# Kernel tuning notes

Measured on AMD Instinct MI355X. Metric: run time of the kernel, lower is better.

Reference implementation:

```python
import jax, jax.numpy as jnp
import numpy as np

B, L, FEAT = 128, 64, 2048   # batch, num image regions, cnn feature dim
T = 48                        # max_seq_len
EMB, UNITS, VOCAB = 256, 512, 5000


def setup_inputs() -> dict:
    key = jax.random.key(0)
    ks = jax.random.split(key, 16)
    s = 0.02
    inp = {
        "img_tensor": jax.random.normal(ks[0], (B, L, FEAT), dtype=jnp.float32),
        "target": jax.random.randint(ks[1], (B, T), 0, VOCAB, dtype=jnp.int32),
        # CNN_Encoder fc: 2048 -> 256
        "W_fc": jax.random.normal(ks[2], (FEAT, EMB), dtype=jnp.float32) * s,
        "b_fc": jnp.zeros((EMB,), jnp.float32),
        # BahdanauAttention
        "W1": jax.random.normal(ks[3], (EMB, UNITS), dtype=jnp.float32) * s,
        "b1": jnp.zeros((UNITS,), jnp.float32),
        "W2": jax.random.normal(ks[4], (UNITS, UNITS), dtype=jnp.float32) * s,
        "b2": jnp.zeros((UNITS,), jnp.float32),
        "V": jax.random.normal(ks[5], (UNITS, 1), dtype=jnp.float32) * s,
        "bV": jnp.zeros((1,), jnp.float32),
        # Decoder embedding
        "emb": jax.random.normal(ks[6], (VOCAB, EMB), dtype=jnp.float32) * s,
        # Keras GRU (reset_after=True): input dim = EMB + UNITS? no: concat(context EMB=256, emb 256) = 512
        "gru_k": jax.random.normal(ks[7], (EMB + EMB, 3 * UNITS), dtype=jnp.float32) * s,
        "gru_rk": jax.random.normal(ks[8], (UNITS, 3 * UNITS), dtype=jnp.float32) * s,
        "gru_b": jnp.zeros((2, 3 * UNITS), jnp.float32),
        # fc1: units->units, fc2: units->vocab
        "fc1_w": jax.random.normal(ks[9], (UNITS, UNITS), dtype=jnp.float32) * s,
        "fc1_b": jnp.zeros((UNITS,), jnp.float32),
        "fc2_w": jax.random.normal(ks[10], (UNITS, VOCAB), dtype=jnp.float32) * s,
        "fc2_b": jnp.zeros((VOCAB,), jnp.float32),
    }
    return inp


def reference(img_tensor, target, W_fc, b_fc, W1, b1, W2, b2, V, bV, emb,
              gru_k, gru_rk, gru_b, fc1_w, fc1_b, fc2_w, fc2_b):
    # CNN encoder: (B, L, EMB)
    features = jax.nn.relu(jnp.einsum('blf,fe->ble', img_tensor, W_fc) + b_fc)
    # Precompute W1(features): invariant across timesteps
    feat_w1 = jnp.einsum('ble,eu->blu', features, W1) + b1  # (B, L, UNITS)

    def step(carry, tok_next):
        hidden, tok = carry
        # Bahdanau attention
        hid_w2 = hidden @ W2 + b2                         # (B, UNITS)
        score = jnp.tanh(feat_w1 + hid_w2[:, None, :])    # (B, L, UNITS)
        logits_attn = jnp.einsum('blu,uo->blo', score, V) + bV  # (B, L, 1)
        attn = jax.nn.softmax(logits_attn, axis=1)
        context = jnp.sum(attn * features, axis=1)        # (B, EMB)
        # Embed previous token, concat with context (seq len 1)
        x = jnp.concatenate([context, emb[tok]], axis=-1)  # (B, 2*EMB)
        # GRU step. NOTE: the original TF code calls self.gru(x) with NO
        # initial_state, so the GRU state is zeros at every timestep.
        h0 = jnp.zeros_like(hidden)
        mx = x @ gru_k + gru_b[0]                          # (B, 3U)
        mh = h0 @ gru_rk + gru_b[1]                        # (B, 3U)
        xz, xr, xh = jnp.split(mx, 3, axis=-1)
        rz, rr, rh = jnp.split(mh, 3, axis=-1)
        z = jax.nn.sigmoid(xz + rz)
        r = jax.nn.sigmoid(xr + rr)
        hh = jnp.tanh(xh + r * rh)
        state = z * h0 + (1.0 - z) * hh                    # (B, UNITS)
        # fc1 -> fc2 logits
        out = state @ fc1_w + fc1_b
        logits = out @ fc2_w + fc2_b                       # (B, VOCAB)
        return (state, tok_next), logits

    batch = target.shape[0]
    hidden0 = jnp.zeros((batch, UNITS), dtype=features.dtype)
    tok0 = jnp.ones((batch,), dtype=target.dtype)          # start token id 1
    xs = jnp.transpose(target[:, 1:], (1, 0))              # (T-1, B)
    _, logits_t = jax.lax.scan(step, (hidden0, tok0), xs)  # (T-1, B, VOCAB)
    return jnp.transpose(logits_t, (1, 0, 2))              # (B, T-1, VOCAB)
```

## Files before the change

kernel.cpp:

```cpp
#include <hip/hip_runtime.h>

typedef __attribute__((ext_vector_type(8))) short short8;
typedef __attribute__((ext_vector_type(4))) float f32x4;

__device__ __forceinline__ float bf2f(ushort u) {
  union { unsigned int i; float f; } x; x.i = ((unsigned int)u) << 16; return x.f;
}
__device__ __forceinline__ ushort f2bf(float f) {
  union { float f; unsigned int i; } x; x.f = f;
  unsigned int i = x.i + 0x7fffu + ((x.i >> 16) & 1u);
  return (ushort)(i >> 16);
}
__device__ __forceinline__ float blo(unsigned int u) {
  union { unsigned int i; float f; } x; x.i = u << 16; return x.f;
}
__device__ __forceinline__ float bhi(unsigned int u) {
  union { unsigned int i; float f; } x; x.i = u & 0xffff0000u; return x.f;
}
__device__ __forceinline__ float fast_tanh(float x) {
  x = fminf(fmaxf(x, -15.f), 15.f);
  float e = __expf(2.f * x);
  return __fdividef(e - 1.f, e + 1.f);
}
__device__ __forceinline__ float sigm(float x) { return 1.f / (1.f + __expf(-x)); }

__global__ void transpose_f2b(const float* __restrict__ in, ushort* __restrict__ out,
                              int R, int C) {
  __shared__ ushort tile[32][33];
  int c0 = blockIdx.x * 32, r0 = blockIdx.y * 32;
  int tx = threadIdx.x, ty = threadIdx.y;
  for (int i = 0; i < 32; i += 8) {
    int r = r0 + ty + i, c = c0 + tx;
    if (r < R && c < C) tile[ty + i][tx] = f2bf(in[(size_t)r * C + c]);
  }
  __syncthreads();
  for (int i = 0; i < 32; i += 8) {
    int c = c0 + ty + i, r = r0 + tx;
    if (r < R && c < C) out[(size_t)c * R + r] = tile[tx][ty + i];
  }
}

__global__ void embed_gather(const int* __restrict__ target, const float* __restrict__ emb,
                             ushort* __restrict__ embA) {
  int m = blockIdx.x;
  int t = m >> 7, b = m & 127;
  int tok = (t == 0) ? 1 : target[b * 48 + t];
  embA[(size_t)m * 256 + threadIdx.x] = f2bf(emb[(size_t)tok * 256 + threadIdx.x]);
}

__global__ __launch_bounds__(256) void gemm128(
    const void* __restrict__ Ap, const ushort* __restrict__ BT,
    const float* __restrict__ bias, void* __restrict__ Cout,
    int M, int N, int K, int NrowsB, int bstride, int flags) {
  __shared__ ushort lA[128 * 32];
  __shared__ ushort lB[128 * 32];
  int tid = threadIdx.x;
  int wave = tid >> 6, lane = tid & 63;
  int q = lane >> 4, l16 = lane & 15;
  int wr = wave >> 1, wc = wave & 1;
  int m0 = blockIdx.y * 128, n0 = blockIdx.x * 128;
  f32x4 acc[4][4];
#pragma unroll
  for (int i = 0; i < 4; ++i)
#pragma unroll
    for (int j = 0; j < 4; ++j) acc[i][j] = (f32x4){0.f, 0.f, 0.f, 0.f};
  int r0 = tid >> 2, cc0 = (tid & 3) * 8;
  int r1 = r0 + 64, cc1 = cc0;
  int rb0 = n0 + r0; if (rb0 >= NrowsB) rb0 = NrowsB - 1;
  int rb1 = n0 + r1; if (rb1 >= NrowsB) rb1 = NrowsB - 1;
  for (int k = 0; k < K; k += 32) {
    short8 va0, va1, vb0, vb1;
    if (flags & 8) {
      const float* s0 = (const float*)Ap + (size_t)(m0 + r0) * K + k + cc0;
      const float* s1 = (const float*)Ap + (size_t)(m0 + r1) * K + k + cc1;
      short8 t0, t1;
#pragma unroll
      for (int e = 0; e < 8; ++e) { t0[e] = (short)f2bf(s0[e]); t1[e] = (short)f2bf(s1[e]); }
      va0 = t0; va1 = t1;
    } else {
      va0 = *(const short8*)((const ushort*)Ap + (size_t)(m0 + r0) * K + k + cc0);
      va1 = *(const short8*)((const ushort*)Ap + (size_t)(m0 + r1) * K + k + cc1);
    }
    vb0 = *(const short8*)(BT + (size_t)rb0 * bstride + k + cc0);
    vb1 = *(const short8*)(BT + (size_t)rb1 * bstride + k + cc1);
    __syncthreads();
    *(short8*)&lA[r0 * 32 + cc0] = va0;
    *(short8*)&lA[r1 * 32 + cc1] = va1;
    *(short8*)&lB[r0 * 32 + cc0] = vb0;
    *(short8*)&lB[r1 * 32 + cc1] = vb1;
    __syncthreads();
    short8 af[4], bfr[4];
#pragma unroll
    for (int i = 0; i < 4; ++i)
      af[i] = *(const short8*)&lA[(wr * 64 + i * 16 + l16) * 32 + q * 8];
#pragma unroll
    for (int j = 0; j < 4; ++j)
      bfr[j] = *(const short8*)&lB[(wc * 64 + j * 16 + l16) * 32 + q * 8];
#pragma unroll
    for (int i = 0; i < 4; ++i)
#pragma unroll
      for (int j = 0; j < 4; ++j)
        acc[i][j] = __builtin_amdgcn_mfma_f32_16x16x32_bf16(af[i], bfr[j], acc[i][j], 0, 0, 0);
  }
#pragma unroll
  for (int i = 0; i < 4; ++i)
#pragma unroll
    for (int j = 0; j < 4; ++j)
#pragma unroll
      for (int r = 0; r < 4; ++r) {
        int gr = m0 + wr * 64 + i * 16 + q * 4 + r;
        int gc = n0 + wc * 64 + j * 16 + l16;
        if (gc >= N) continue;
        float v = acc[i][j][r];
        if (bias) v += bias[gc];
        if (flags & 1) v = fmaxf(v, 0.f);
        size_t orow = (size_t)gr;
        if (flags & 4) { int t = gr >> 7, bb = gr & 127; orow = (size_t)bb * 47 + t; }
        if (flags & 2) ((float*)Cout)[orow * (size_t)N + gc] = v;
        else ((ushort*)Cout)[orow * (size_t)N + gc] = f2bf(v);
      }
}

__global__ __launch_bounds__(512) void row_loop(
    const ushort* __restrict__ featW1,
    const ushort* __restrict__ W2T,
    const float* __restrict__ b2,
    const float* __restrict__ V,
    const float* __restrict__ bV,
    const ushort* __restrict__ featK,
    const ushort* __restrict__ xE,
    const float* __restrict__ grub0,
    const float* __restrict__ grub1,
    ushort* __restrict__ states) {
  int b = blockIdx.x, tid = threadIdx.x;
  __shared__ __align__(16) float stf[512];
  __shared__ float hw2p[520], Vvp[520];
  __shared__ float sc[64], attnw[64];
  float b2r = b2[tid];
  float g0z = grub0[tid], g0r = grub0[512 + tid], g0h = grub0[1024 + tid];
  float g1z = grub1[tid], g1r = grub1[512 + tid], g1h = grub1[1024 + tid];
  float bVr = bV[0];
  Vvp[tid + (tid >> 6)] = V[tid];
  stf[tid] = 0.f;
  const uint4* w2row = (const uint4*)(W2T + (size_t)tid * 512);
  int l = tid >> 3, part = tid & 7;
  const short8* fw8 = (const short8*)(featW1 + ((size_t)(b * 64 + l)) * 512 + part * 64);
  const ushort* fkb = featK + (size_t)b * 64 * 1536 + tid;
  __syncthreads();

#pragma unroll 1
  for (int t = 0; t < 47; ++t) {
    {
      float s0 = 0.f, s1 = 0.f;
#pragma unroll 8
      for (int k8 = 0; k8 < 64; ++k8) {
        uint4 w = w2row[k8];
        const float4* sp = (const float4*)(stf + k8 * 8);
        float4 sA = sp[0], sB = sp[1];
        s0 += blo(w.x) * sA.x + bhi(w.x) * sA.y;
        s1 += blo(w.y) * sA.z + bhi(w.y) * sA.w;
        s0 += blo(w.z) * sB.x + bhi(w.z) * sB.y;
        s1 += blo(w.w) * sB.z + bhi(w.w) * sB.w;
      }
      hw2p[tid + (tid >> 6)] = s0 + s1 + b2r;
    }
    __syncthreads();
    {
      float s = 0.f;
#pragma unroll 2
      for (int u8 = 0; u8 < 8; ++u8) {
        short8 fv = fw8[u8];
        int ub = part * 64 + u8 * 8;
        int pi = ub + part;
#pragma unroll
        for (int e = 0; e < 8; ++e) {
          float x = bf2f((ushort)fv[e]) + hw2p[pi + e];
          s += fast_tanh(x) * Vvp[pi + e];
        }
      }
      s += __shfl_xor(s, 1);
      s += __shfl_xor(s, 2);
      s += __shfl_xor(s, 4);
      if (part == 0) sc[l] = s + bVr;
    }
    __syncthreads();
    if (tid < 64) {
      float v = sc[tid], m = v;
      for (int o = 32; o; o >>= 1) m = fmaxf(m, __shfl_xor(m, o));
      float e = __expf(v - m), ss = e;
      for (int o = 32; o; o >>= 1) ss += __shfl_xor(ss, o);
      attnw[tid] = e / ss;
    }
    __syncthreads();
    {
      const ushort* xe = xE + ((size_t)(t * 128 + b)) * 1536;
      float az = bf2f(xe[tid]), ar = bf2f(xe[512 + tid]), ah = bf2f(xe[1024 + tid]);
      const ushort* fk = fkb;
#pragma unroll 4
      for (int l2 = 0; l2 < 64; ++l2) {
        float a = attnw[l2];
        az += a * bf2f(fk[0]);
        ar += a * bf2f(fk[512]);
        ah += a * bf2f(fk[1024]);
        fk += 1536;
      }
      float z = sigm(az + g0z + g1z);
      float r = sigm(ar + g0r + g1r);
      float hh = fast_tanh(ah + g0h + r * g1h);
      float st = (1.f - z) * hh;
      stf[tid] = st;
      states[((size_t)(t + 1) * 128 + b) * 512 + tid] = f2bf(st);
    }
    __syncthreads();
  }
}

extern "C" void kernel_launch(void* const* d_in, const int* in_sizes, int n_in,
                              void* d_out, int out_size, void* d_ws, size_t ws_size,
                              hipStream_t stream) {
  const float* img    = (const float*)d_in[0];
  const int*   target = (const int*)d_in[1];
  const float* W_fc   = (const float*)d_in[2];
  const float* b_fc   = (const float*)d_in[3];
  const float* W1     = (const float*)d_in[4];
  const float* b1     = (const float*)d_in[5];
  const float* W2     = (const float*)d_in[6];
  const float* b2     = (const float*)d_in[7];
  const float* V      = (const float*)d_in[8];
  const float* bV     = (const float*)d_in[9];
  const float* emb    = (const float*)d_in[10];
  const float* gru_k  = (const float*)d_in[11];
  const float* gru_b  = (const float*)d_in[13];
  const float* fc1_w  = (const float*)d_in[14];
  const float* fc1_b  = (const float*)d_in[15];
  const float* fc2_w  = (const float*)d_in[16];
  const float* fc2_b  = (const float*)d_in[17];

  char* wsb = (char*)d_ws;
  size_t off = 0;
  auto alloc = [&](size_t bytes) {
    char* p = wsb + off;
    off += (bytes + 255) & ~(size_t)255;
    return p;
  };
  ushort* W_fcT  = (ushort*)alloc((size_t)256 * 2048 * 2);
  ushort* W1T    = (ushort*)alloc((size_t)512 * 256 * 2);
  ushort* W2T    = (ushort*)alloc((size_t)512 * 512 * 2);
  ushort* gruT   = (ushort*)alloc((size_t)1536 * 512 * 2);
  ushort* fc1T   = (ushort*)alloc((size_t)512 * 512 * 2);
  ushort* fc2T   = (ushort*)alloc((size_t)5000 * 512 * 2);
  ushort* hid2ws = (ushort*)alloc((size_t)6016 * 512 * 2);

  char* ob = (char*)d_out;
  ushort* features = (ushort*)(ob);
  ushort* featW1   = (ushort*)(ob + (size_t)4194304);
  ushort* states   = (ushort*)(ob + (size_t)12582912);
  ushort* embA     = (ushort*)(ob + (size_t)18874368);
  ushort* featK    = (ushort*)(ob + (size_t)21954560);
  ushort* xE       = (ushort*)(ob + (size_t)47120384);

  dim3 tb(32, 8);
  transpose_f2b<<<dim3(8, 64), tb, 0, stream>>>(W_fc, W_fcT, 2048, 256);
  transpose_f2b<<<dim3(16, 8), tb, 0, stream>>>(W1, W1T, 256, 512);
  transpose_f2b<<<dim3(16, 16), tb, 0, stream>>>(W2, W2T, 512, 512);
  transpose_f2b<<<dim3(48, 16), tb, 0, stream>>>(gru_k, gruT, 512, 1536);
  transpose_f2b<<<dim3(16, 16), tb, 0, stream>>>(fc1_w, fc1T, 512, 512);
  transpose_f2b<<<dim3(157, 16), tb, 0, stream>>>(fc2_w, fc2T, 512, 5000);

  embed_gather<<<6016, 256, 0, stream>>>(target, emb, embA);

  gemm128<<<dim3(2, 64), 256, 0, stream>>>(img, W_fcT, b_fc, features,
                                           8192, 256, 2048, 256, 2048, 1 | 8);
  gemm128<<<dim3(4, 64), 256, 0, stream>>>(features, W1T, b1, featW1,
                                           8192, 512, 256, 512, 256, 0);
  gemm128<<<dim3(12, 64), 256, 0, stream>>>(features, gruT, nullptr, featK,
                                            8192, 1536, 256, 1536, 512, 0);
  gemm128<<<dim3(12, 47), 256, 0, stream>>>(embA, gruT + 256, nullptr, xE,
                                            6016, 1536, 256, 1536, 512, 0);

  row_loop<<<128, 512, 0, stream>>>(featW1, W2T, b2, V, bV, featK, xE,
                                    gru_b, gru_b + 1536, states);

  gemm128<<<dim3(4, 47), 256, 0, stream>>>(states + (size_t)128 * 512, fc1T, fc1_b,
                                           hid2ws, 6016, 512, 512, 512, 512, 0);
  gemm128<<<dim3(40, 47), 256, 0, stream>>>(hid2ws, fc2T, fc2_b, d_out,
                                            6016, 5000, 512, 5000, 512, 2 | 4);
}
```

Baseline: 1.757 ms.

## Compute context vector then apply GRU kernel instead of precomputing featK

Removes the large features·gru_k GEMM (8192x1536) and its 25MB intermediate. Instead, the recurrent kernel computes the attention-weighted context over features held in shared memory, then multiplies that 256-vector by the GRU input weights on each step. This trades a big precomputed GEMM and its per-step strided featK reads for a per-step 256x1536 matvec inside the sequential loop, which lengthens the critical path. It also adds about 65KB of shared memory per block.

```diff
diff --git a/kernel.cpp b/kernel.cpp
--- a/kernel.cpp
+++ b/kernel.cpp
@@ -123,29 +123,40 @@
 
 __global__ __launch_bounds__(512) void row_loop(
     const ushort* __restrict__ featW1,
+    const ushort* __restrict__ features,
     const ushort* __restrict__ W2T,
     const float* __restrict__ b2,
     const float* __restrict__ V,
     const float* __restrict__ bV,
-    const ushort* __restrict__ featK,
+    const ushort* __restrict__ gruT,
     const ushort* __restrict__ xE,
     const float* __restrict__ grub0,
     const float* __restrict__ grub1,
     ushort* __restrict__ states) {
   int b = blockIdx.x, tid = threadIdx.x;
   __shared__ __align__(16) float stf[512];
+  __shared__ __align__(16) float lctx[256];
   __shared__ float hw2p[520], Vvp[520];
   __shared__ float sc[64], attnw[64];
+  __shared__ float featsT[256][65];
   float b2r = b2[tid];
   float g0z = grub0[tid], g0r = grub0[512 + tid], g0h = grub0[1024 + tid];
   float g1z = grub1[tid], g1r = grub1[512 + tid], g1h = grub1[1024 + tid];
   float bVr = bV[0];
   Vvp[tid + (tid >> 6)] = V[tid];
   stf[tid] = 0.f;
+  {
+    int k = tid & 255;
+    for (int l = tid >> 8; l < 64; l += 2)
+      featsT[k][l] = bf2f(features[(size_t)(b * 64 + l) * 256 + k]);
+  }
   const uint4* w2row = (const uint4*)(W2T + (size_t)tid * 512);
+  const uint4* gz = (const uint4*)(gruT + (size_t)tid * 512);
+  const uint4* gr = (const uint4*)(gruT + (size_t)(512 + tid) * 512);
+  const uint4* gh = (const uint4*)(gruT + (size_t)(1024 + tid) * 512);
   int l = tid >> 3, part = tid & 7;
   const short8* fw8 = (const short8*)(featW1 + ((size_t)(b * 64 + l)) * 512 + part * 64);
-  const ushort* fkb = featK + (size_t)b * 64 * 1536 + tid;
+  int kc = tid >> 1, hc = tid & 1;
   __syncthreads();
 
 #pragma unroll 1
@@ -193,16 +204,41 @@
     }
     __syncthreads();
     {
-      const ushort* xe = xE + ((size_t)(t * 128 + b)) * 1536;
-      float az = bf2f(xe[tid]), ar = bf2f(xe[512 + tid]), ah = bf2f(xe[1024 + tid]);
-      const ushort* fk = fkb;
+      float s = 0.f;
+      const float* fr = &featsT[kc][hc * 32];
+      const float* aw = attnw + hc * 32;
+#pragma unroll 8
+      for (int l2 = 0; l2 < 32; ++l2) s += aw[l2] * fr[l2];
+      s += __shfl_xor(s, 1);
+      if (hc == 0) lctx[kc] = s;
+    }
+    __syncthreads();
+    {
+      const ushort* xe = xE + ((size_t)(t * 128 + b)) * 1536 + tid;
+      float az = bf2f(xe[0]), ar = bf2f(xe[512]), ah = bf2f(xe[1024]);
 #pragma unroll 4
-      for (int l2 = 0; l2 < 64; ++l2) {
-        float a = attnw[l2];
-        az += a * bf2f(fk[0]);
-        ar += a * bf2f(fk[512]);
-        ah += a * bf2f(fk[1024]);
-        fk += 1536;
+      for (int k8 = 0; k8 < 32; ++k8) {
+        uint4 w = gz[k8];
+        const float4* cp = (const float4*)(lctx + k8 * 8);
+        float4 cA = cp[0], cB = cp[1];
+        az += blo(w.x) * cA.x + bhi(w.x) * cA.y + blo(w.y) * cA.z + bhi(w.y) * cA.w +
+              blo(w.z) * cB.x + bhi(w.z) * cB.y + blo(w.w) * cB.z + bhi(w.w) * cB.w;
+      }
+#pragma unroll 4
+      for (int k8 = 0; k8 < 32; ++k8) {
+        uint4 w = gr[k8];
+        const float4* cp = (const float4*)(lctx + k8 * 8);
+        float4 cA = cp[0], cB = cp[1];
+        ar += blo(w.x) * cA.x + bhi(w.x) * cA.y + blo(w.y) * cA.z + bhi(w.y) * cA.w +
+              blo(w.z) * cB.x + bhi(w.z) * cB.y + blo(w.w) * cB.z + bhi(w.w) * cB.w;
+      }
+#pragma unroll 4
+      for (int k8 = 0; k8 < 32; ++k8) {
+        uint4 w = gh[k8];
+        const float4* cp = (const float4*)(lctx + k8 * 8);
+        float4 cA = cp[0], cB = cp[1];
+        ah += blo(w.x) * cA.x + bhi(w.x) * cA.y + blo(w.y) * cA.z + bhi(w.y) * cA.w +
+              blo(w.z) * cB.x + bhi(w.z) * cB.y + blo(w.w) * cB.z + bhi(w.w) * cB.w;
       }
       float z = sigm(az + g0z + g1z);
       float r = sigm(ar + g0r + g1r);
@@ -256,8 +292,7 @@
   ushort* featW1   = (ushort*)(ob + (size_t)4194304);
   ushort* states   = (ushort*)(ob + (size_t)12582912);
   ushort* embA     = (ushort*)(ob + (size_t)18874368);
-  ushort* featK    = (ushort*)(ob + (size_t)21954560);
-  ushort* xE       = (ushort*)(ob + (size_t)47120384);
+  ushort* xE       = (ushort*)(ob + (size_t)21954560);
 
   dim3 tb(32, 8);
   transpose_f2b<<<dim3(8, 64), tb, 0, stream>>>(W_fc, W_fcT, 2048, 256);
@@ -273,13 +308,11 @@
                                            8192, 256, 2048, 256, 2048, 1 | 8);
   gemm128<<<dim3(4, 64), 256, 0, stream>>>(features, W1T, b1, featW1,
                                            8192, 512, 256, 512, 256, 0);
-  gemm128<<<dim3(12, 64), 256, 0, stream>>>(features, gruT, nullptr, featK,
-                                            8192, 1536, 256, 1536, 512, 0);
   gemm128<<<dim3(12, 47), 256, 0, stream>>>(embA, gruT + 256, nullptr, xE,
                                             6016, 1536, 256, 1536, 512, 0);
 
-  row_loop<<<128, 512, 0, stream>>>(featW1, W2T, b2, V, bV, featK, xE,
-                                    gru_b, gru_b + 1536, states);
+  row_loop<<<128, 512, 0, stream>>>(featW1, features, W2T, b2, V, bV,
+                                    gruT, xE, gru_b, gru_b + 1536, states);
 
   gemm128<<<dim3(4, 47), 256, 0, stream>>>(states + (size_t)128 * 512, fc1T, fc1_b,
                                            hid2ws, 6016, 512, 512, 512, 512, 0);
```

New measurement: 2.468 ms. +40.5%, slower.

## Split each batch row's recurrent loop across a pair of cooperating blocks

Applied to the files above, without the earlier changes.

The sequential attention+GRU loop now runs two blocks per batch element, each owning half of the hidden units. Partial attention scores and state halves are exchanged through global memory with agent-scope atomics and flag spin-waits, launched cooperatively so all 256 blocks are co-resident. It also keeps W2 and featW1 slices in registers and a transposed featK slice in LDS, cutting global reloads per timestep. The cost is two cross-block handshakes per step and heavy register and LDS use, which could stall the loop if latency dominates.

```diff
diff --git a/kernel.cpp b/kernel.cpp
--- a/kernel.cpp
+++ b/kernel.cpp
@@ -23,6 +23,12 @@
   return __fdividef(e - 1.f, e + 1.f);
 }
 __device__ __forceinline__ float sigm(float x) { return 1.f / (1.f + __expf(-x)); }
+__device__ __forceinline__ void st_agent(float* p, float v) {
+  __hip_atomic_store(p, v, __ATOMIC_RELAXED, __HIP_MEMORY_SCOPE_AGENT);
+}
+__device__ __forceinline__ float ld_agent(const float* p) {
+  return __hip_atomic_load(p, __ATOMIC_RELAXED, __HIP_MEMORY_SCOPE_AGENT);
+}
 
 __global__ void transpose_f2b(const float* __restrict__ in, ushort* __restrict__ out,
                               int R, int C) {
@@ -121,7 +127,7 @@
       }
 }
 
-__global__ __launch_bounds__(512) void row_loop(
+__global__ __launch_bounds__(512, 2) void row_pair(
     const ushort* __restrict__ featW1,
     const ushort* __restrict__ W2T,
     const float* __restrict__ b2,
@@ -131,61 +137,137 @@
     const ushort* __restrict__ xE,
     const float* __restrict__ grub0,
     const float* __restrict__ grub1,
-    ushort* __restrict__ states) {
-  int b = blockIdx.x, tid = threadIdx.x;
-  __shared__ __align__(16) float stf[512];
-  __shared__ float hw2p[520], Vvp[520];
-  __shared__ float sc[64], attnw[64];
-  float b2r = b2[tid];
-  float g0z = grub0[tid], g0r = grub0[512 + tid], g0h = grub0[1024 + tid];
-  float g1z = grub1[tid], g1r = grub1[512 + tid], g1h = grub1[1024 + tid];
+    ushort* __restrict__ states,
+    float* __restrict__ stateF,
+    float* __restrict__ scG,
+    int* __restrict__ flagA,
+    int* __restrict__ flagB) {
+  int bid = blockIdx.x, tid = threadIdx.x;
+  int h = (bid >> 3) & 1;
+  int b = (bid & 7) * 16 + (bid >> 4);
+  int ph = 1 - h;
+  int fown = b * 2 + h, fpar = b * 2 + ph;
+
+  __shared__ __align__(16) ushort fkT[768][64];
+  __shared__ __align__(16) float stf_p[544];
+  __shared__ float hw2p[264], Vvp[264];
+  __shared__ float scOwn[64], attnw[64];
+  __shared__ float xbuf[768];
+
+  if (tid < 256) Vvp[tid + (tid >> 5)] = V[h * 256 + tid];
+  for (int i = tid; i < 544; i += 512) stf_p[i] = 0.f;
+  {
+    int w = tid >> 6, lane = tid & 63;
+    for (int l = w; l < 64; l += 8) {
+      const ushort* src = featK + (size_t)(b * 64 + l) * 1536;
+      for (int c = lane; c < 768; c += 64) {
+        int gc = (c >> 8) * 512 + h * 256 + (c & 255);
+        fkT[c][l] = src[gc];
+      }
+    }
+  }
+  int hk = tid & 7, up = tid >> 3;
+  uint4 wreg[32];
+#pragma unroll
+  for (int i = 0; i < 4; ++i)
+#pragma unroll
+    for (int m = 0; m < 8; ++m)
+      wreg[i * 8 + m] = *(const uint4*)(W2T + (size_t)(h * 256 + up * 4 + i) * 512 + hk * 64 + m * 8);
+  float b2v0 = b2[h * 256 + up * 4], b2v1 = b2[h * 256 + up * 4 + 1];
+  float b2v2 = b2[h * 256 + up * 4 + 2], b2v3 = b2[h * 256 + up * 4 + 3];
+  int lr = tid >> 3, part = tid & 7;
+  uint4 fwreg[4];
+#pragma unroll
+  for (int i = 0; i < 4; ++i)
+    fwreg[i] = *(const uint4*)(featW1 + (size_t)(b * 64 + lr) * 512 + h * 256 + part * 32 + i * 8);
+  float g0z = 0, g0r = 0, g0h = 0, g1z = 0, g1r = 0, g1h = 0;
+  if (tid < 256) {
+    int gu = h * 256 + tid;
+    g0z = grub0[gu]; g0r = grub0[512 + gu]; g0h = grub0[1024 + gu];
+    g1z = grub1[gu]; g1r = grub1[512 + gu]; g1h = grub1[1024 + gu];
+  }
   float bVr = bV[0];
-  Vvp[tid + (tid >> 6)] = V[tid];
-  stf[tid] = 0.f;
-  const uint4* w2row = (const uint4*)(W2T + (size_t)tid * 512);
-  int l = tid >> 3, part = tid & 7;
-  const short8* fw8 = (const short8*)(featW1 + ((size_t)(b * 64 + l)) * 512 + part * 64);
-  const ushort* fkb = featK + (size_t)b * 64 * 1536 + tid;
   __syncthreads();
 
 #pragma unroll 1
   for (int t = 0; t < 47; ++t) {
+    const ushort* xerow = xE + (size_t)(t * 128 + b) * 1536;
+    ushort xe1 = xerow[(tid >> 8) * 512 + h * 256 + (tid & 255)];
+    ushort xe2 = (tid < 256) ? xerow[1024 + h * 256 + tid] : (ushort)0;
+    if (t > 0) {
+      if (tid == 0) {
+        while (atomicAdd(&flagB[fpar], 0) < t) __builtin_amdgcn_s_sleep(2);
+      }
+      __syncthreads();
+      __threadfence();
+      if (tid < 256) {
+        int gu = ph * 256 + tid;
+        stf_p[gu + (gu >> 6) * 4] =
+            ld_agent(&stateF[(size_t)(t & 1) * 65536 + (size_t)b * 512 + gu]);
+      }
+    }
+    __syncthreads();
     {
-      float s0 = 0.f, s1 = 0.f;
-#pragma unroll 8
-      for (int k8 = 0; k8 < 64; ++k8) {
-        uint4 w = w2row[k8];
-        const float4* sp = (const float4*)(stf + k8 * 8);
-        float4 sA = sp[0], sB = sp[1];
-        s0 += blo(w.x) * sA.x + bhi(w.x) * sA.y;
-        s1 += blo(w.y) * sA.z + bhi(w.y) * sA.w;
-        s0 += blo(w.z) * sB.x + bhi(w.z) * sB.y;
-        s1 += blo(w.w) * sB.z + bhi(w.w) * sB.w;
-      }
-      hw2p[tid + (tid >> 6)] = s0 + s1 + b2r;
+      float a0 = 0, a1 = 0, a2 = 0, a3 = 0;
+      const float* sb = &stf_p[hk * 68];
+#pragma unroll
+      for (int m = 0; m < 8; ++m) {
+        float4 sA = *(const float4*)(sb + m * 8);
+        float4 sB = *(const float4*)(sb + m * 8 + 4);
+        uint4 w0 = wreg[m], w1 = wreg[8 + m], w2 = wreg[16 + m], w3 = wreg[24 + m];
+        a0 += blo(w0.x) * sA.x + bhi(w0.x) * sA.y + blo(w0.y) * sA.z + bhi(w0.y) * sA.w +
+              blo(w0.z) * sB.x + bhi(w0.z) * sB.y + blo(w0.w) * sB.z + bhi(w0.w) * sB.w;
+        a1 += blo(w1.x) * sA.x + bhi(w1.x) * sA.y + blo(w1.y) * sA.z + bhi(w1.y) * sA.w +
+              blo(w1.z) * sB.x + bhi(w1.z) * sB.y + blo(w1.w) * sB.z + bhi(w1.w) * sB.w;
+        a2 += blo(w2.x) * sA.x + bhi(w2.x) * sA.y + blo(w2.y) * sA.z + bhi(w2.y) * sA.w +
+              blo(w2.z) * sB.x + bhi(w2.z) * sB.y + blo(w2.w) * sB.z + bhi(w2.w) * sB.w;
+        a3 += blo(w3.x) * sA.x + bhi(w3.x) * sA.y + blo(w3.y) * sA.z + bhi(w3.y) * sA.w +
+              blo(w3.z) * sB.x + bhi(w3.z) * sB.y + blo(w3.w) * sB.z + bhi(w3.w) * sB.w;
+      }
+      a0 += __shfl_xor(a0, 1); a0 += __shfl_xor(a0, 2); a0 += __shfl_xor(a0, 4);
+      a1 += __shfl_xor(a1, 1); a1 += __shfl_xor(a1, 2); a1 += __shfl_xor(a1, 4);
+      a2 += __shfl_xor(a2, 1); a2 += __shfl_xor(a2, 2); a2 += __shfl_xor(a2, 4);
+      a3 += __shfl_xor(a3, 1); a3 += __shfl_xor(a3, 2); a3 += __shfl_xor(a3, 4);
+      if (hk == 0) {
+        int u0 = up * 4, pad = (u0 >> 5);
+        hw2p[u0 + pad] = a0 + b2v0;
+        hw2p[u0 + 1 + pad] = a1 + b2v1;
+        hw2p[u0 + 2 + pad] = a2 + b2v2;
+        hw2p[u0 + 3 + pad] = a3 + b2v3;
+      }
     }
     __syncthreads();
     {
       float s = 0.f;
-#pragma unroll 2
-      for (int u8 = 0; u8 < 8; ++u8) {
-        short8 fv = fw8[u8];
-        int ub = part * 64 + u8 * 8;
-        int pi = ub + part;
+      int pib = part * 33;
+#pragma unroll
+      for (int i = 0; i < 4; ++i) {
+        uint4 fv = fwreg[i];
+        const ushort* fu = (const ushort*)&fv;
+        int base = pib + i * 8;
 #pragma unroll
         for (int e = 0; e < 8; ++e) {
-          float x = bf2f((ushort)fv[e]) + hw2p[pi + e];
-          s += fast_tanh(x) * Vvp[pi + e];
+          float x = bf2f(fu[e]) + hw2p[base + e];
+          s += fast_tanh(x) * Vvp[base + e];
         }
       }
-      s += __shfl_xor(s, 1);
-      s += __shfl_xor(s, 2);
-      s += __shfl_xor(s, 4);
-      if (part == 0) sc[l] = s + bVr;
-    }
-    __syncthreads();
+      s += __shfl_xor(s, 1); s += __shfl_xor(s, 2); s += __shfl_xor(s, 4);
+      if (part == 0) {
+        scOwn[lr] = s;
+        st_agent(&scG[(size_t)fown * 64 + lr], s);
+      }
+    }
+    __syncthreads();
+    if (tid == 0) {
+      __threadfence();
+      atomicExch(&flagA[fown], t + 1);
+      while (atomicAdd(&flagA[fpar], 0) < t + 1) __builtin_amdgcn_s_sleep(2);
+    }
+    __syncthreads();
+    __threadfence();
     if (tid < 64) {
-      float v = sc[tid], m = v;
+      float v = scOwn[tid] + ld_agent(&scG[(size_t)fpar * 64 + tid]) + bVr;
+      float m = v;
       for (int o = 32; o; o >>= 1) m = fmaxf(m, __shfl_xor(m, o));
       float e = __expf(v - m), ss = e;
       for (int o = 32; o; o >>= 1) ss += __shfl_xor(ss, o);
@@ -193,25 +275,50 @@
     }
     __syncthreads();
     {
-      const ushort* xe = xE + ((size_t)(t * 128 + b)) * 1536;
-      float az = bf2f(xe[tid]), ar = bf2f(xe[512 + tid]), ah = bf2f(xe[1024 + tid]);
-      const ushort* fk = fkb;
-#pragma unroll 4
-      for (int l2 = 0; l2 < 64; ++l2) {
-        float a = attnw[l2];
-        az += a * bf2f(fk[0]);
-        ar += a * bf2f(fk[512]);
-        ah += a * bf2f(fk[1024]);
-        fk += 1536;
-      }
-      float z = sigm(az + g0z + g1z);
-      float r = sigm(ar + g0r + g1r);
-      float hh = fast_tanh(ah + g0h + r * g1h);
+      int j = tid;
+      float x1 = bf2f(xe1);
+#pragma unroll
+      for (int s8 = 0; s8 < 8; ++s8) {
+        int p = s8 ^ (j & 7);
+        uint4 v = *(const uint4*)&fkT[j][p * 8];
+        const ushort* vu = (const ushort*)&v;
+        const float* aw = &attnw[p * 8];
+#pragma unroll
+        for (int e = 0; e < 8; ++e) x1 += aw[e] * bf2f(vu[e]);
+      }
+      xbuf[j] = x1;
+      if (tid < 256) {
+        int j2 = 512 + tid;
+        float x2 = bf2f(xe2);
+#pragma unroll
+        for (int s8 = 0; s8 < 8; ++s8) {
+          int p = s8 ^ (j2 & 7);
+          uint4 v = *(const uint4*)&fkT[j2][p * 8];
+          const ushort* vu = (const ushort*)&v;
+          const float* aw = &attnw[p * 8];
+#pragma unroll
+          for (int e = 0; e < 8; ++e) x2 += aw[e] * bf2f(vu[e]);
+        }
+        xbuf[j2] = x2;
+      }
+    }
+    __syncthreads();
+    if (tid < 256) {
+      float xz = xbuf[tid], xr = xbuf[256 + tid], xh = xbuf[512 + tid];
+      float z = sigm(xz + g0z + g1z);
+      float r = sigm(xr + g0r + g1r);
+      float hh = fast_tanh(xh + g0h + r * g1h);
       float st = (1.f - z) * hh;
-      stf[tid] = st;
-      states[((size_t)(t + 1) * 128 + b) * 512 + tid] = f2bf(st);
-    }
-    __syncthreads();
+      int gu = h * 256 + tid;
+      stf_p[gu + (gu >> 6) * 4] = st;
+      states[((size_t)(t + 1) * 128 + b) * 512 + gu] = f2bf(st);
+      st_agent(&stateF[(size_t)((t + 1) & 1) * 65536 + (size_t)b * 512 + gu], st);
+    }
+    __syncthreads();
+    if (tid == 0) {
+      __threadfence();
+      atomicExch(&flagB[fown], t + 1);
+    }
   }
 }
 
@@ -250,6 +357,9 @@
   ushort* fc1T   = (ushort*)alloc((size_t)512 * 512 * 2);
   ushort* fc2T   = (ushort*)alloc((size_t)5000 * 512 * 2);
   ushort* hid2ws = (ushort*)alloc((size_t)6016 * 512 * 2);
+  float*  stateF = (float*)alloc((size_t)2 * 128 * 512 * 4);
+  float*  scG    = (float*)alloc((size_t)128 * 2 * 64 * 4);
+  int*    flags  = (int*)alloc((size_t)512 * 4);
 
   char* ob = (char*)d_out;
   ushort* features = (ushort*)(ob);
@@ -278,8 +388,17 @@
   gemm128<<<dim3(12, 47), 256, 0, stream>>>(embA, gruT + 256, nullptr, xE,
                                             6016, 1536, 256, 1536, 512, 0);
 
-  row_loop<<<128, 512, 0, stream>>>(featW1, W2T, b2, V, bV, featK, xE,
-                                    gru_b, gru_b + 1536, states);
+  hipMemsetAsync(flags, 0, 512 * sizeof(int), stream);
+
+  {
+    const ushort *a0 = featW1, *a1 = W2T, *a5 = featK, *a6 = xE;
+    const float *a2 = b2, *a3 = V, *a4 = bV, *a7 = gru_b, *a8 = gru_b + 1536;
+    ushort* a9 = states;
+    float *a10 = stateF, *a11 = scG;
+    int *a12 = flags, *a13 = flags + 256;
+    void* kargs[] = {&a0, &a1, &a2, &a3, &a4, &a5, &a6, &a7, &a8, &a9, &a10, &a11, &a12, &a13};
+    hipLaunchCooperativeKernel((void*)row_pair, dim3(256), dim3(512), kargs, 0, stream);
+  }
 
   gemm128<<<dim3(4, 47), 256, 0, stream>>>(states + (size_t)128 * 512, fc1T, fc1_b,
                                            hid2ws, 6016, 512, 512, 512, 512, 0);
```

Result: slower. 5.819 ms (+231.2%).
